# Kernel optimization log

Measured on AMD Instinct MI355X. Metric: run time of the kernel, lower is better.

Reference implementation:

```python
import jax, jax.numpy as jnp
import numpy as np

TEMPERATURE = 0.05
EPS = 1e-8  # matches torch F.cosine_similarity eps default


def setup_inputs() -> dict:
    key = jax.random.key(0)
    k1, k2 = jax.random.split(key)
    N, D = 8192, 512
    query_embeddings = jax.random.normal(k1, (N, D), dtype=jnp.float32)
    pos_embeddings = jax.random.normal(k2, (N, D), dtype=jnp.float32)
    return {"query_embeddings": query_embeddings, "pos_embeddings": pos_embeddings}


def reference(query_embeddings, pos_embeddings):
    # cosine_similarity(q[:,None,:], p[None,:,:], dim=2) == normalize(q) @ normalize(p).T
    qn = query_embeddings / jnp.maximum(
        jnp.linalg.norm(query_embeddings, axis=-1, keepdims=True), EPS)
    pn = pos_embeddings / jnp.maximum(
        jnp.linalg.norm(pos_embeddings, axis=-1, keepdims=True), EPS)
    sim = jnp.einsum('nd,md->nm', qn, pn) / TEMPERATURE  # [N, N] logits
    # cross-entropy with targets = arange(N): diagonal logits are the positives
    logz = jax.nn.logsumexp(sim, axis=-1)               # [N]
    diag = jnp.diagonal(sim)                             # [N]
    loss = jnp.mean(logz - diag)
    return loss
```

## Files before the change

kernel.cpp:

```cpp
#include <hip/hip_runtime.h>
#include <hip/hip_bf16.h>

#define NROWS 8192
#define DIM 512
#define BM 256
#define BN 256

typedef int   i32x4 __attribute__((ext_vector_type(4)));
typedef int   i32x8 __attribute__((ext_vector_type(8)));
typedef float f32x4 __attribute__((ext_vector_type(4)));

#define FP8_SCALE_1 0x7f7f7f7f

__global__ __launch_bounds__(256) void prep_k(
    const float* __restrict__ q, const float* __restrict__ p,
    char* __restrict__ qf, char* __restrict__ pf,
    float* __restrict__ diag) {
  __shared__ char ldsq[16 * 528];
  __shared__ char ldsp[16 * 528];
  const int tid = threadIdx.x;
  const int blk = blockIdx.x;
  const int rr = tid >> 4;
  const int cs = tid & 15;
  const int i  = blk * 16 + rr;
  const float4* qr = (const float4*)(q + (size_t)i * DIM);
  const float4* pr = (const float4*)(p + (size_t)i * DIM);

  float4 qv[8], pv[8];
  float ssq = 0.0f, ssp = 0.0f, dt = 0.0f;
  #pragma unroll
  for (int jj = 0; jj < 8; ++jj) {
    qv[jj] = qr[jj * 16 + cs];
    pv[jj] = pr[jj * 16 + cs];
    ssq += qv[jj].x*qv[jj].x + qv[jj].y*qv[jj].y + qv[jj].z*qv[jj].z + qv[jj].w*qv[jj].w;
    ssp += pv[jj].x*pv[jj].x + pv[jj].y*pv[jj].y + pv[jj].z*pv[jj].z + pv[jj].w*pv[jj].w;
    dt  += qv[jj].x*pv[jj].x + qv[jj].y*pv[jj].y + qv[jj].z*pv[jj].z + qv[jj].w*pv[jj].w;
  }
  #pragma unroll
  for (int m = 1; m < 16; m <<= 1) {
    ssq += __shfl_xor(ssq, m, 64);
    ssp += __shfl_xor(ssp, m, 64);
    dt  += __shfl_xor(dt,  m, 64);
  }
  const float invq = 1.0f / fmaxf(sqrtf(ssq), 1e-8f);
  const float invp = 1.0f / fmaxf(sqrtf(ssp), 1e-8f);
  if (cs == 0) diag[i] = dt * invq * invp * 20.0f;

  #pragma unroll
  for (int jj = 0; jj < 8; ++jj) {
    int rq = 0, rp = 0;
    rq = __builtin_amdgcn_cvt_pk_fp8_f32(qv[jj].x * invq, qv[jj].y * invq, rq, false);
    rq = __builtin_amdgcn_cvt_pk_fp8_f32(qv[jj].z * invq, qv[jj].w * invq, rq, true);
    rp = __builtin_amdgcn_cvt_pk_fp8_f32(pv[jj].x * invp, pv[jj].y * invp, rp, false);
    rp = __builtin_amdgcn_cvt_pk_fp8_f32(pv[jj].z * invp, pv[jj].w * invp, rp, true);
    *(unsigned int*)(ldsq + rr * 528 + jj * 64 + cs * 4) = (unsigned int)rq;
    *(unsigned int*)(ldsp + rr * 528 + jj * 64 + cs * 4) = (unsigned int)rp;
  }
  __syncthreads();

  const int panel = blk >> 4, rg = blk & 15;
  #pragma unroll
  for (int u = 0; u < 2; ++u) {
    const int o = 2 * tid + u;
    const int kt = o >> 7, sel = (o >> 6) & 1, laneT = o & 63;
    const int rrs = laneT & 15;
    const int srcoff = kt * 128 + (laneT >> 4) * 32 + sel * 16;
    const i32x4 va = *(const i32x4*)(ldsq + rrs * 528 + srcoff);
    const size_t aaddr =
        ((((size_t)(panel * 4 + kt) * 2 + (rg >> 3)) * 8 + (rg & 7)) * 2 + sel) * 1024
        + laneT * 16;
    *(i32x4*)(qf + aaddr) = va;
    const i32x4 vb = *(const i32x4*)(ldsp + rrs * 528 + srcoff);
    const size_t baddr =
        ((((size_t)(panel * 4 + kt) * 4 + (rg >> 2)) * 4 + (rg & 3)) * 2 + sel) * 1024
        + laneT * 16;
    *(i32x4*)(pf + baddr) = vb;
  }
}

__global__ __launch_bounds__(512, 2) void gemm_lse_k(
    const char* __restrict__ qf, const char* __restrict__ pf,
    float* __restrict__ partial) {
  __shared__ float psum[1024];
  const int tid = threadIdx.x;
  const int lane = tid & 63, wid = tid >> 6;
  const int wr = wid >> 2, wc = wid & 3;
  const int l15 = lane & 15, l4 = lane >> 4;
  const int b = blockIdx.x;
  const int g = b & 7;
  const int j = b >> 3;
  const int panelA = (g & 3) * 8 + (j & 7);
  const int bnset  = (g >> 2) * 16 + (j >> 3) * 4;
  const int bm = panelA * BM;
  const char* aPanel = qf + (size_t)panelA * 131072 + (size_t)lane * 16;
  const char* pBase  = pf + (size_t)lane * 16;

  f32x4 acc[4][8] = {};
  i32x8 af[8], bf[4];

  #pragma unroll 1
  for (int tt = 0; tt < 16; ++tt) {
    const int kt = tt & 3, t = tt >> 2;
    const char* aB = aPanel + (size_t)(kt * 2 + wr) * 16384;
    const char* bB = pBase +
        (size_t)(((bnset + t) * 4 + kt) * 4 + wc) * 8192;

    #pragma unroll
    for (int mf = 0; mf < 8; ++mf) {
      const i32x4 lo = *(const i32x4*)(aB + mf * 2048);
      const i32x4 hi = *(const i32x4*)(aB + mf * 2048 + 1024);
      af[mf] = __builtin_shufflevector(lo, hi, 0, 1, 2, 3, 4, 5, 6, 7);
    }
    #pragma unroll
    for (int nf = 0; nf < 4; ++nf) {
      const i32x4 lo = *(const i32x4*)(bB + nf * 2048);
      const i32x4 hi = *(const i32x4*)(bB + nf * 2048 + 1024);
      bf[nf] = __builtin_shufflevector(lo, hi, 0, 1, 2, 3, 4, 5, 6, 7);
    }

    __builtin_amdgcn_s_setprio(1);
    #pragma unroll
    for (int nb = 0; nb < 4; ++nb)
      #pragma unroll
      for (int am = 0; am < 8; ++am)
        acc[nb][am] = __builtin_amdgcn_mfma_scale_f32_16x16x128_f8f6f4(
            bf[nb], af[am], acc[nb][am], 0, 0, 0, FP8_SCALE_1, 0, FP8_SCALE_1);
    __builtin_amdgcn_s_setprio(0);

    if ((tt & 3) == 3) {
      const int bxc = bnset + t;
      #pragma unroll
      for (int am = 0; am < 8; ++am) {
        float s = 0.0f;
        #pragma unroll
        for (int nb = 0; nb < 4; ++nb)
          #pragma unroll
          for (int r = 0; r < 4; ++r)
            s += __expf(acc[nb][am][r] * 20.0f - 20.0f);
        s += __shfl_xor(s, 16, 64);
        s += __shfl_xor(s, 32, 64);
        if (l4 == 0)
          psum[wc * 256 + wr * 128 + am * 16 + l15] = s;
      }
      __syncthreads();
      if (tid < 256)
        partial[(size_t)(bm + tid) * 32 + bxc] =
            psum[tid] + psum[256 + tid] + psum[512 + tid] + psum[768 + tid];
      __syncthreads();
      #pragma unroll
      for (int nb = 0; nb < 4; ++nb)
        #pragma unroll
        for (int am = 0; am < 8; ++am)
          acc[nb][am] = f32x4{0.0f, 0.0f, 0.0f, 0.0f};
    }
  }
}

__global__ __launch_bounds__(256) void rowloss_k(
    const float* __restrict__ partial, const float* __restrict__ diag,
    float* __restrict__ rowloss) {
  const int i = blockIdx.x * 256 + threadIdx.x;
  const float4* pr = (const float4*)(partial + (size_t)i * 32);
  float s = 0.0f;
  #pragma unroll
  for (int c = 0; c < 8; ++c) {
    const float4 v = pr[c];
    s += v.x + v.y + v.z + v.w;
  }
  rowloss[i] = __logf(s) + 20.0f - diag[i];
}

__global__ __launch_bounds__(1024) void final_k(
    const float* __restrict__ rowloss, float* __restrict__ out) {
  const int t = threadIdx.x;
  float s = 0.0f;
  #pragma unroll
  for (int j = 0; j < 8; ++j) s += rowloss[t + j * 1024];
  #pragma unroll
  for (int m = 1; m < 64; m <<= 1) s += __shfl_xor(s, m, 64);
  __shared__ float red[16];
  if ((t & 63) == 0) red[t >> 6] = s;
  __syncthreads();
  if (t == 0) {
    float acc = 0.0f;
    #pragma unroll
    for (int w = 0; w < 16; ++w) acc += red[w];
    out[0] = acc * (1.0f / (float)NROWS);
  }
}

extern "C" void kernel_launch(void* const* d_in, const int* in_sizes, int n_in,
                              void* d_out, int out_size, void* d_ws, size_t ws_size,
                              hipStream_t stream) {
  const float* q = (const float*)d_in[0];
  const float* p = (const float*)d_in[1];
  char* w = (char*)d_ws;
  char* qf = w;
  char* pf = w + 4194304;
  float* partial    = (float*)(w + 8388608);
  float* diag       = (float*)(w + 9437184);
  float* rowloss    = (float*)(w + 9437184 + 32768);
  float* out = (float*)d_out;

  prep_k<<<NROWS / 16, 256, 0, stream>>>(q, p, qf, pf, diag);
  gemm_lse_k<<<256, 512, 0, stream>>>(qf, pf, partial);
  rowloss_k<<<NROWS / 256, 256, 0, stream>>>(partial, diag, rowloss);
  final_k<<<1, 1024, 0, stream>>>(rowloss, out);
}
```

Measured before the change: 57.33 us.

## Switch FP8 GEMM to 32x32x64 scaled MFMA with matching operand layout

Replaces the 16x16x128 scaled FP8 MFMA tiles with 32x32x64 tiles, which means fewer, larger MFMA instructions per wave. The prep kernel now handles 32 rows per block and writes a new fragment layout shared by Q and P, and the LSE epilogue is adapted to the 16-element accumulators. The larger MFMA shape is meant to raise matrix-core throughput and reduce instruction issue overhead. The price is heavier per-lane accumulator and epilogue work, plus the risk that the new layout mapping is wrong.

After: 58.21 us. About the same (+1.5%).

```diff
diff --git a/kernel.cpp b/kernel.cpp
--- a/kernel.cpp
+++ b/kernel.cpp
@@ -9,20 +9,21 @@
 typedef int   i32x4 __attribute__((ext_vector_type(4)));
 typedef int   i32x8 __attribute__((ext_vector_type(8)));
 typedef float f32x4 __attribute__((ext_vector_type(4)));
+typedef float f32x16 __attribute__((ext_vector_type(16)));
 
 #define FP8_SCALE_1 0x7f7f7f7f
 
-__global__ __launch_bounds__(256) void prep_k(
+__global__ __launch_bounds__(512) void prep_k(
     const float* __restrict__ q, const float* __restrict__ p,
     char* __restrict__ qf, char* __restrict__ pf,
     float* __restrict__ diag) {
-  __shared__ char ldsq[16 * 528];
-  __shared__ char ldsp[16 * 528];
+  __shared__ char ldsq[32 * 528];
+  __shared__ char ldsp[32 * 528];
   const int tid = threadIdx.x;
   const int blk = blockIdx.x;
   const int rr = tid >> 4;
   const int cs = tid & 15;
-  const int i  = blk * 16 + rr;
+  const int i  = blk * 32 + rr;
   const float4* qr = (const float4*)(q + (size_t)i * DIM);
   const float4* pr = (const float4*)(p + (size_t)i * DIM);
 
@@ -58,23 +59,17 @@
   }
   __syncthreads();
 
-  const int panel = blk >> 4, rg = blk & 15;
+  const int panel = blk >> 3, grp = blk & 7;
   #pragma unroll
   for (int u = 0; u < 2; ++u) {
     const int o = 2 * tid + u;
-    const int kt = o >> 7, sel = (o >> 6) & 1, laneT = o & 63;
-    const int rrs = laneT & 15;
-    const int srcoff = kt * 128 + (laneT >> 4) * 32 + sel * 16;
-    const i32x4 va = *(const i32x4*)(ldsq + rrs * 528 + srcoff);
-    const size_t aaddr =
-        ((((size_t)(panel * 4 + kt) * 2 + (rg >> 3)) * 8 + (rg & 7)) * 2 + sel) * 1024
-        + laneT * 16;
-    *(i32x4*)(qf + aaddr) = va;
-    const i32x4 vb = *(const i32x4*)(ldsp + rrs * 528 + srcoff);
-    const size_t baddr =
-        ((((size_t)(panel * 4 + kt) * 4 + (rg >> 2)) * 4 + (rg & 3)) * 2 + sel) * 1024
-        + laneT * 16;
-    *(i32x4*)(pf + baddr) = vb;
+    const int kf = o >> 7, sel = (o >> 6) & 1, laneT = o & 63;
+    const int rrs = laneT & 31;
+    const int srcoff = kf * 64 + (laneT >> 5) * 32 + sel * 16;
+    const size_t addr =
+        (((size_t)(panel * 8 + kf) * 8 + grp) * 2048) + sel * 1024 + laneT * 16;
+    *(i32x4*)(qf + addr) = *(const i32x4*)(ldsq + rrs * 528 + srcoff);
+    *(i32x4*)(pf + addr) = *(const i32x4*)(ldsp + rrs * 528 + srcoff);
   }
 }
 
@@ -85,62 +80,68 @@
   const int tid = threadIdx.x;
   const int lane = tid & 63, wid = tid >> 6;
   const int wr = wid >> 2, wc = wid & 3;
-  const int l15 = lane & 15, l4 = lane >> 4;
+  const int l31 = lane & 31;
   const int b = blockIdx.x;
   const int g = b & 7;
   const int j = b >> 3;
   const int panelA = (g & 3) * 8 + (j & 7);
   const int bnset  = (g >> 2) * 16 + (j >> 3) * 4;
   const int bm = panelA * BM;
-  const char* aPanel = qf + (size_t)panelA * 131072 + (size_t)lane * 16;
-  const char* pBase  = pf + (size_t)lane * 16;
-
-  f32x4 acc[4][8] = {};
-  i32x8 af[8], bf[4];
+  const char* aBase = qf + (size_t)panelA * 131072 + (size_t)lane * 16;
+  const char* pBase = pf + (size_t)lane * 16;
+
+  f32x16 acc[2][4] = {};
+  i32x8 af[4][2], bf[2][2];
 
   #pragma unroll 1
   for (int tt = 0; tt < 16; ++tt) {
     const int kt = tt & 3, t = tt >> 2;
-    const char* aB = aPanel + (size_t)(kt * 2 + wr) * 16384;
-    const char* bB = pBase +
-        (size_t)(((bnset + t) * 4 + kt) * 4 + wc) * 8192;
-
-    #pragma unroll
-    for (int mf = 0; mf < 8; ++mf) {
-      const i32x4 lo = *(const i32x4*)(aB + mf * 2048);
-      const i32x4 hi = *(const i32x4*)(aB + mf * 2048 + 1024);
-      af[mf] = __builtin_shufflevector(lo, hi, 0, 1, 2, 3, 4, 5, 6, 7);
-    }
-    #pragma unroll
-    for (int nf = 0; nf < 4; ++nf) {
-      const i32x4 lo = *(const i32x4*)(bB + nf * 2048);
-      const i32x4 hi = *(const i32x4*)(bB + nf * 2048 + 1024);
-      bf[nf] = __builtin_shufflevector(lo, hi, 0, 1, 2, 3, 4, 5, 6, 7);
-    }
+
+    #pragma unroll
+    for (int am = 0; am < 4; ++am)
+      #pragma unroll
+      for (int ks = 0; ks < 2; ++ks) {
+        const char* fa = aBase + (size_t)((kt * 2 + ks) * 8 + wr * 4 + am) * 2048;
+        const i32x4 lo = *(const i32x4*)(fa);
+        const i32x4 hi = *(const i32x4*)(fa + 1024);
+        af[am][ks] = __builtin_shufflevector(lo, hi, 0, 1, 2, 3, 4, 5, 6, 7);
+      }
+    #pragma unroll
+    for (int nb = 0; nb < 2; ++nb)
+      #pragma unroll
+      for (int ks = 0; ks < 2; ++ks) {
+        const char* fb = pBase +
+            (size_t)(((bnset + t) * 8 + kt * 2 + ks) * 8 + wc * 2 + nb) * 2048;
+        const i32x4 lo = *(const i32x4*)(fb);
+        const i32x4 hi = *(const i32x4*)(fb + 1024);
+        bf[nb][ks] = __builtin_shufflevector(lo, hi, 0, 1, 2, 3, 4, 5, 6, 7);
+      }
 
     __builtin_amdgcn_s_setprio(1);
     #pragma unroll
-    for (int nb = 0; nb < 4; ++nb)
-      #pragma unroll
-      for (int am = 0; am < 8; ++am)
-        acc[nb][am] = __builtin_amdgcn_mfma_scale_f32_16x16x128_f8f6f4(
-            bf[nb], af[am], acc[nb][am], 0, 0, 0, FP8_SCALE_1, 0, FP8_SCALE_1);
+    for (int nb = 0; nb < 2; ++nb)
+      #pragma unroll
+      for (int am = 0; am < 4; ++am)
+        #pragma unroll
+        for (int ks = 0; ks < 2; ++ks)
+          acc[nb][am] = __builtin_amdgcn_mfma_scale_f32_32x32x64_f8f6f4(
+              bf[nb][ks], af[am][ks], acc[nb][am], 0, 0,
+              0, FP8_SCALE_1, 0, FP8_SCALE_1);
     __builtin_amdgcn_s_setprio(0);
 
     if ((tt & 3) == 3) {
       const int bxc = bnset + t;
       #pragma unroll
-      for (int am = 0; am < 8; ++am) {
+      for (int am = 0; am < 4; ++am) {
         float s = 0.0f;
         #pragma unroll
-        for (int nb = 0; nb < 4; ++nb)
+        for (int nb = 0; nb < 2; ++nb)
           #pragma unroll
-          for (int r = 0; r < 4; ++r)
+          for (int r = 0; r < 16; ++r)
             s += __expf(acc[nb][am][r] * 20.0f - 20.0f);
-        s += __shfl_xor(s, 16, 64);
         s += __shfl_xor(s, 32, 64);
-        if (l4 == 0)
-          psum[wc * 256 + wr * 128 + am * 16 + l15] = s;
+        if (lane < 32)
+          psum[wc * 256 + wr * 128 + am * 32 + l31] = s;
       }
       __syncthreads();
       if (tid < 256)
@@ -148,10 +149,11 @@
             psum[tid] + psum[256 + tid] + psum[512 + tid] + psum[768 + tid];
       __syncthreads();
       #pragma unroll
-      for (int nb = 0; nb < 4; ++nb)
+      for (int nb = 0; nb < 2; ++nb)
         #pragma unroll
-        for (int am = 0; am < 8; ++am)
-          acc[nb][am] = f32x4{0.0f, 0.0f, 0.0f, 0.0f};
+        for (int am = 0; am < 4; ++am)
+          acc[nb][am] = f32x16{0.0f, 0.0f, 0.0f, 0.0f, 0.0f, 0.0f, 0.0f, 0.0f,
+                               0.0f, 0.0f, 0.0f, 0.0f, 0.0f, 0.0f, 0.0f, 0.0f};
     }
   }
 }
@@ -202,7 +204,7 @@
   float* rowloss    = (float*)(w + 9437184 + 32768);
   float* out = (float*)d_out;
 
-  prep_k<<<NROWS / 16, 256, 0, stream>>>(q, p, qf, pf, diag);
+  prep_k<<<NROWS / 32, 512, 0, stream>>>(q, p, qf, pf, diag);
   gemm_lse_k<<<256, 512, 0, stream>>>(qf, pf, partial);
   rowloss_k<<<NROWS / 256, 256, 0, stream>>>(partial, diag, rowloss);
   final_k<<<1, 1024, 0, stream>>>(rowloss, out);
```
